# Kernel optimization log

Hardware: AMD Instinct MI355X
Metric: run time of the kernel (lower is better)

Reference implementation:

```python
import jax, jax.numpy as jnp
import numpy as np

SIGMA_S = 1.0
SIGMA_R = 0.1
FR = int(np.ceil(3 * SIGMA_S))          # 3
K_SIZE = 2 * FR + 1                     # 7
B, C, H, W = 8, 3, 512, 512


def matlab_style_gauss2d(shape, sigma):
    m, n = [(ss - 1.0) / 2.0 for ss in shape]
    y, x = np.ogrid[-m:m + 1, -n:n + 1]
    h = np.exp(-(x * x + y * y) / (2.0 * sigma * sigma))
    h[h < np.finfo(h.dtype).eps * h.max()] = 0
    s = h.sum()
    if s != 0:
        h /= s
    return h.astype(np.float32)


GAUSS = matlab_style_gauss2d((K_SIZE, K_SIZE), SIGMA_S)  # [7,7]


def setup_inputs() -> dict:
    key = jax.random.key(0)
    x = jax.random.uniform(key, (B, C, H, W), dtype=jnp.float32)
    return {"input": x}


def reference(input) -> jnp.ndarray:
    # ReflectionPad2d(fr)
    padded = jnp.pad(input, ((0, 0), (0, 0), (FR, FR), (FR, FR)), mode="reflect")
    inv_2sr2 = 1.0 / (2.0 * SIGMA_R * SIGMA_R)
    loss_map = jnp.zeros_like(input)
    for k in range(K_SIZE):
        for l in range(K_SIZE):
            shifted = padded[:, :, k:k + H, l:l + W]            # [B,C,H,W]
            d = input - shifted
            # bilateral range weight * gaussian spatial weight (constant, as in
            # the original which stores weight_map as a raw non-grad tensor)
            w = jax.lax.stop_gradient(
                jnp.exp(-(d * d).sum(1, keepdims=True) * inv_2sr2) * GAUSS[k, l]
            )                                                    # [B,1,H,W]
            loss_map = loss_map + jnp.abs(d) * w
    return loss_map.mean()
```

## Files before the change

### kernel.cpp

```cpp
#include <hip/hip_runtime.h>

#define FR 3
#define KS 7
#define TILE 32
#define HALO (TILE + 2*FR)
#define LSTR 40
#define IMG_H 512
#define IMG_W 512
#define NB 8
#define NC 3

__device__ __forceinline__ int refl(int i, int n) {
    i = (i < 0) ? -i : i;
    return (i >= n) ? (2*n - 2 - i) : i;
}

__global__ __launch_bounds__(256) void blt_kernel(const float* __restrict__ in,
                                                  float* __restrict__ ws) {
    __shared__ float sm[NC][HALO][LSTR];
    __shared__ float wsum[4];
    const int bx  = blockIdx.x * TILE;
    const int by  = blockIdx.y * TILE;
    const int b   = blockIdx.z;
    const int tx  = threadIdx.x;
    const int tid = threadIdx.y * 32 + tx;
    const float* base = in + (size_t)b * NC * IMG_H * IMG_W;

    for (int idx = tid; idx < HALO * HALO; idx += 256) {
        int ly = idx / HALO;
        int lx = idx - ly * HALO;
        int gy = refl(by + ly - FR, IMG_H);
        int gx = refl(bx + lx - FR, IMG_W);
        #pragma unroll
        for (int c = 0; c < NC; ++c)
            sm[c][ly][lx] = base[(c * IMG_H + gy) * IMG_W + gx];
    }
    __syncthreads();

    constexpr double g0 = 0.011108996538242306;
    constexpr double g1 = 0.1353352832366127;
    constexpr double g2 = 0.6065306597126334;
    constexpr double g1d[7] = {g0, g1, g2, 1.0, g2, g1, g0};
    constexpr double SUMG = 1.0 + 2.0 * (g0 + g1 + g2);
    constexpr double INVS = 1.0 / (SUMG * SUMG);

    float acc = 0.0f;
    #pragma unroll
    for (int i = 0; i < 4; ++i) {
        const int py = threadIdx.y + 8 * i;
        const float c0 = sm[0][py + FR][tx + FR];
        const float c1 = sm[1][py + FR][tx + FR];
        const float c2 = sm[2][py + FR][tx + FR];
        #pragma unroll
        for (int k = 0; k < KS; ++k) {
            #pragma unroll
            for (int l = 0; l < KS; ++l) {
                if (k == FR && l == FR) continue;
                const float wg = (float)(g1d[k] * g1d[l] * INVS);
                float v0 = sm[0][py + k][tx + l];
                float v1 = sm[1][py + k][tx + l];
                float v2 = sm[2][py + k][tx + l];
                float d0 = c0 - v0, d1 = c1 - v1, d2 = c2 - v2;
                float s  = d0 * d0 + d1 * d1 + d2 * d2;
                float w  = __expf(s * -50.0f) * wg;
                acc += (fabsf(d0) + fabsf(d1) + fabsf(d2)) * w;
            }
        }
    }

    #pragma unroll
    for (int off = 32; off > 0; off >>= 1)
        acc += __shfl_down(acc, off, 64);
    const int lane = tid & 63, wid = tid >> 6;
    if (lane == 0) wsum[wid] = acc;
    __syncthreads();
    if (tid == 0)
        atomicAdd(ws, wsum[0] + wsum[1] + wsum[2] + wsum[3]);
}

__global__ void finalize_kernel(const float* __restrict__ ws, float* __restrict__ out) {
    out[0] = ws[0] / (float)(NB * NC * IMG_H * IMG_W);
}

extern "C" void kernel_launch(void* const* d_in, const int* in_sizes, int n_in,
                              void* d_out, int out_size, void* d_ws, size_t ws_size,
                              hipStream_t stream) {
    const float* in = (const float*)d_in[0];
    float* out = (float*)d_out;
    float* ws  = (float*)d_ws;

    hipMemsetAsync(ws, 0, sizeof(float), stream);

    dim3 grid(IMG_W / TILE, IMG_H / TILE, NB);
    dim3 block(32, 8);
    blt_kernel<<<grid, block, 0, stream>>>(in, ws);
    finalize_kernel<<<1, 1, 0, stream>>>(ws, out);
}
```

Measured before the change: 109.1 us.

## Restructure bilateral loss with row-sliding reuse, prescaled exp2, and partial-sum reduction

```diff
diff --git a/kernel.cpp b/kernel.cpp
--- a/kernel.cpp
+++ b/kernel.cpp
@@ -2,13 +2,21 @@
 
 #define FR 3
 #define KS 7
-#define TILE 32
-#define HALO (TILE + 2*FR)
-#define LSTR 40
+#define TLX 64
+#define TLY 16
+#define PPT 4
+#define HX (TLX + 2*FR)
+#define HY (TLY + 2*FR)
+#define LSTR 72
 #define IMG_H 512
 #define IMG_W 512
 #define NB 8
 #define NC 3
+#define GX (IMG_W / TLX)
+#define GY (IMG_H / TLY)
+#define NBLK (GX * GY * NB)
+
+#define KSC 8.493218f
 
 __device__ __forceinline__ int refl(int i, int n) {
     i = (i < 0) ? -i : i;
@@ -16,70 +24,115 @@
 }
 
 __global__ __launch_bounds__(256) void blt_kernel(const float* __restrict__ in,
-                                                  float* __restrict__ ws) {
-    __shared__ float sm[NC][HALO][LSTR];
+                                                  float* __restrict__ partial) {
+    __shared__ float sm[NC][HY][LSTR];
+    __shared__ float gtab[8];
     __shared__ float wsum[4];
-    const int bx  = blockIdx.x * TILE;
-    const int by  = blockIdx.y * TILE;
+
+    constexpr double g0 = 0.011108996538242306;
+    constexpr double g1 = 0.1353352832366127;
+    constexpr double g2 = 0.6065306597126334;
+    constexpr double SUMG = 1.0 + 2.0 * (g0 + g1 + g2);
+    constexpr double KD   = 8.493218;
+    const float glc[KS] = {
+        (float)(g0 / (SUMG * SUMG * KD)), (float)(g1 / (SUMG * SUMG * KD)),
+        (float)(g2 / (SUMG * SUMG * KD)), (float)(1.0 / (SUMG * SUMG * KD)),
+        (float)(g2 / (SUMG * SUMG * KD)), (float)(g1 / (SUMG * SUMG * KD)),
+        (float)(g0 / (SUMG * SUMG * KD))
+    };
+
+    const int bx  = blockIdx.x * TLX;
+    const int by  = blockIdx.y * TLY;
     const int b   = blockIdx.z;
     const int tx  = threadIdx.x;
-    const int tid = threadIdx.y * 32 + tx;
+    const int ty  = threadIdx.y;
+    const int tid = ty * 64 + tx;
     const float* base = in + (size_t)b * NC * IMG_H * IMG_W;
 
-    for (int idx = tid; idx < HALO * HALO; idx += 256) {
-        int ly = idx / HALO;
-        int lx = idx - ly * HALO;
+    if (tid == 0) {
+        gtab[0] = (float)g0; gtab[1] = (float)g1; gtab[2] = (float)g2;
+        gtab[3] = 1.0f;      gtab[4] = (float)g2; gtab[5] = (float)g1;
+        gtab[6] = (float)g0;
+    }
+
+    for (int idx = tid; idx < HY * HX; idx += 256) {
+        int ly = idx / HX;
+        int lx = idx - ly * HX;
         int gy = refl(by + ly - FR, IMG_H);
         int gx = refl(bx + lx - FR, IMG_W);
         #pragma unroll
         for (int c = 0; c < NC; ++c)
-            sm[c][ly][lx] = base[(c * IMG_H + gy) * IMG_W + gx];
+            sm[c][ly][lx] = base[(c * IMG_H + gy) * IMG_W + gx] * KSC;
     }
     __syncthreads();
 
-    constexpr double g0 = 0.011108996538242306;
-    constexpr double g1 = 0.1353352832366127;
-    constexpr double g2 = 0.6065306597126334;
-    constexpr double g1d[7] = {g0, g1, g2, 1.0, g2, g1, g0};
-    constexpr double SUMG = 1.0 + 2.0 * (g0 + g1 + g2);
-    constexpr double INVS = 1.0 / (SUMG * SUMG);
+    const int r0 = ty * PPT;
+    float c0[PPT], c1[PPT], c2[PPT], acc[PPT];
+    #pragma unroll
+    for (int i = 0; i < PPT; ++i) {
+        c0[i] = sm[0][r0 + i + FR][tx + FR];
+        c1[i] = sm[1][r0 + i + FR][tx + FR];
+        c2[i] = sm[2][r0 + i + FR][tx + FR];
+        acc[i] = 0.0f;
+    }
 
-    float acc = 0.0f;
-    #pragma unroll
-    for (int i = 0; i < 4; ++i) {
-        const int py = threadIdx.y + 8 * i;
-        const float c0 = sm[0][py + FR][tx + FR];
-        const float c1 = sm[1][py + FR][tx + FR];
-        const float c2 = sm[2][py + FR][tx + FR];
+    #pragma unroll 1
+    for (int r = 0; r < PPT + KS - 1; ++r) {
+        const int hr = r0 + r;
+        float v0[KS], v1[KS], v2[KS];
         #pragma unroll
-        for (int k = 0; k < KS; ++k) {
+        for (int l = 0; l < KS; ++l) {
+            v0[l] = sm[0][hr][tx + l];
+            v1[l] = sm[1][hr][tx + l];
+            v2[l] = sm[2][hr][tx + l];
+        }
+        #pragma unroll
+        for (int i = 0; i < PPT; ++i) {
+            const int k = r - i;
+            if (k < 0 || k >= KS) continue;
+            float t = 0.0f;
             #pragma unroll
             for (int l = 0; l < KS; ++l) {
-                if (k == FR && l == FR) continue;
-                const float wg = (float)(g1d[k] * g1d[l] * INVS);
-                float v0 = sm[0][py + k][tx + l];
-                float v1 = sm[1][py + k][tx + l];
-                float v2 = sm[2][py + k][tx + l];
-                float d0 = c0 - v0, d1 = c1 - v1, d2 = c2 - v2;
-                float s  = d0 * d0 + d1 * d1 + d2 * d2;
-                float w  = __expf(s * -50.0f) * wg;
-                acc += (fabsf(d0) + fabsf(d1) + fabsf(d2)) * w;
+                float d0 = c0[i] - v0[l];
+                float d1 = c1[i] - v1[l];
+                float d2 = c2[i] - v2[l];
+                float s = d0 * d0;
+                s = fmaf(d1, d1, s);
+                s = fmaf(d2, d2, s);
+                float e = __builtin_amdgcn_exp2f(-s);
+                float sa = fabsf(d0) + fabsf(d1);
+                sa += fabsf(d2);
+                t = fmaf(sa, e * glc[l], t);
             }
+            acc[i] = fmaf(t, gtab[k], acc[i]);
         }
     }
 
+    float a = acc[0] + acc[1] + acc[2] + acc[3];
     #pragma unroll
     for (int off = 32; off > 0; off >>= 1)
-        acc += __shfl_down(acc, off, 64);
-    const int lane = tid & 63, wid = tid >> 6;
-    if (lane == 0) wsum[wid] = acc;
+        a += __shfl_down(a, off, 64);
+    if ((tid & 63) == 0) wsum[tid >> 6] = a;
+    __syncthreads();
+    if (tid == 0) {
+        int bid = blockIdx.x + GX * (blockIdx.y + GY * blockIdx.z);
+        partial[bid] = wsum[0] + wsum[1] + wsum[2] + wsum[3];
+    }
+}
+
+__global__ __launch_bounds__(256) void finalize_kernel(const float* __restrict__ partial,
+                                                       float* __restrict__ out) {
+    __shared__ float wsum[4];
+    const int tid = threadIdx.x;
+    float a = 0.0f;
+    for (int i = tid; i < NBLK; i += 256) a += partial[i];
+    #pragma unroll
+    for (int off = 32; off > 0; off >>= 1)
+        a += __shfl_down(a, off, 64);
+    if ((tid & 63) == 0) wsum[tid >> 6] = a;
     __syncthreads();
     if (tid == 0)
-        atomicAdd(ws, wsum[0] + wsum[1] + wsum[2] + wsum[3]);
-}
-
-__global__ void finalize_kernel(const float* __restrict__ ws, float* __restrict__ out) {
-    out[0] = ws[0] / (float)(NB * NC * IMG_H * IMG_W);
+        out[0] = (wsum[0] + wsum[1] + wsum[2] + wsum[3]) / (float)(NB * NC * IMG_H * IMG_W);
 }
 
 extern "C" void kernel_launch(void* const* d_in, const int* in_sizes, int n_in,
@@ -89,10 +142,8 @@
     float* out = (float*)d_out;
     float* ws  = (float*)d_ws;
 
-    hipMemsetAsync(ws, 0, sizeof(float), stream);
-
-    dim3 grid(IMG_W / TILE, IMG_H / TILE, NB);
-    dim3 block(32, 8);
+    dim3 grid(GX, GY, NB);
+    dim3 block(TLX, 256 / TLX);
     blt_kernel<<<grid, block, 0, stream>>>(in, ws);
-    finalize_kernel<<<1, 1, 0, stream>>>(ws, out);
+    finalize_kernel<<<1, 256, 0, stream>>>(ws, out);
 }
```

Measured after the change: 107.2 us. Within noise of the previous version (-1.7%).
